# Performance work log

Hardware: AMD Instinct MI355X
Metric: run time of the kernel (lower is better)

The kernel has to match this reference:

```python
import jax, jax.numpy as jnp
import numpy as np

RADIUS = 400.0
FIELD = 8000.0  # um extent of slide coordinate field


def setup_inputs() -> dict:
    key = jax.random.key(0)
    ks = jax.random.split(key, 8)
    B, N, D, H, K = 4, 4096, 1536, 512, 8
    images = jax.random.normal(ks[0], (B, N, D), dtype=jnp.float32)
    positions = jax.random.uniform(ks[1], (B, N, 2), dtype=jnp.float32) * FIELD
    W_feat = jax.random.normal(ks[2], (D, H), dtype=jnp.float32) * (1.0 / np.sqrt(D))
    b_feat = jnp.zeros((H,), dtype=jnp.float32)
    W_pos = jax.random.normal(ks[3], (2, H), dtype=jnp.float32) * 0.5
    W_gnn = jax.random.normal(ks[4], (H, H), dtype=jnp.float32) * (1.0 / np.sqrt(H))
    W_self = jax.random.normal(ks[5], (H, H), dtype=jnp.float32) * (1.0 / np.sqrt(H))
    anchors = jax.random.normal(ks[6], (K, D), dtype=jnp.float32)
    return {"images": images, "positions": positions, "W_feat": W_feat,
            "b_feat": b_feat, "W_pos": W_pos, "W_gnn": W_gnn,
            "W_self": W_self, "anchors": anchors}


def _radius_adjacency(pos):
    # pos: (N, 2). Dense O(N^2) radius graph (mirrors torch.cdist + mask).
    sq = jnp.sum(pos * pos, axis=-1)                       # (N,)
    d2 = sq[:, None] + sq[None, :] - 2.0 * (pos @ pos.T)   # (N, N)
    mask = d2 < (RADIUS * RADIUS)
    N = pos.shape[0]
    mask = mask & ~jnp.eye(N, dtype=bool)                  # no self-loops
    return mask.astype(pos.dtype)


def reference(images, positions, W_feat, b_feat, W_pos, W_gnn, W_self, anchors):
    # --- Stream A: explicit concept quantifier (cosine sim to anchors) ---
    x_norm = images / jnp.clip(jnp.linalg.norm(images, axis=-1, keepdims=True), 1e-12)
    a_norm = anchors / jnp.clip(jnp.linalg.norm(anchors, axis=-1, keepdims=True), 1e-12)
    scores = jnp.einsum('bnd,kd->bnk', x_norm, a_norm)     # (B, N, K)
    concept_profile = scores.mean(axis=1)                  # (B, K)

    # --- Stream B: feature extraction with positional encoding ---
    feat = images @ W_feat + b_feat + positions @ W_pos    # (B, N, H)

    # --- radius graph + one mean-aggregation GNN layer, per slide ---
    def per_graph(f, p):
        A = _radius_adjacency(p)                           # (N, N)
        deg = jnp.clip(A.sum(axis=-1, keepdims=True), 1.0) # (N, 1)
        h = jax.nn.relu(f)
        agg = (A @ h) / deg                                # mean over neighbors
        return jax.nn.relu(agg @ W_gnn + f @ W_self)       # (N, H)

    refined = jax.vmap(per_graph)(feat, positions)         # (B, N, H)
    latent_spatial = refined.mean(axis=1)                  # (B, H)  per-graph mean pool

    return jnp.concatenate([latent_spatial, concept_profile], axis=1)  # (B, H+K)
```

## Files before the change

kernel.cpp:

```cpp
#include <hip/hip_runtime.h>

#define B_ 4
#define N_ 4096
#define D_ 1536
#define H_ 512
#define K_ 8
#define M_ (B_*N_)
#define R2_ 160000.0f
#define CAP 192

typedef __attribute__((ext_vector_type(8))) short bf16x8;
typedef __attribute__((ext_vector_type(4))) float f32x4;

__device__ __forceinline__ unsigned short f2bf(float f) {
  union { float f; unsigned u; } v; v.f = f;
  unsigned r = (v.u + 0x7FFFu + ((v.u >> 16) & 1u)) >> 16;
  return (unsigned short)r;
}

typedef const __attribute__((address_space(1))) unsigned int gas_u32;
typedef __attribute__((address_space(3))) unsigned int las_u32;
__device__ __forceinline__ void gl_lds16(const unsigned short* g, unsigned short* l) {
  __builtin_amdgcn_global_load_lds((gas_u32*)g, (las_u32*)l, 16, 0, 0);
}

__global__ __launch_bounds__(256) void k_prep(
    const float* __restrict__ Wf, const float* __restrict__ Wg, const float* __restrict__ Ws,
    const float* __restrict__ anchors, unsigned short* __restrict__ WfT,
    unsigned short* __restrict__ WgsT, float* __restrict__ anorm) {
  __shared__ float t[64][65];
  __shared__ float red[4];
  int bx = blockIdx.x, by = blockIdx.y, tid = threadIdx.x;
  if (by == 40) {
    int k = bx;
    float s = 0.f;
    for (int i = tid; i < D_; i += 256) { float v = anchors[k*D_ + i]; s += v*v; }
    #pragma unroll
    for (int off = 32; off; off >>= 1) s += __shfl_down(s, off);
    if ((tid & 63) == 0) red[tid >> 6] = s;
    __syncthreads();
    if (tid == 0) anorm[k] = fmaxf(sqrtf(red[0]+red[1]+red[2]+red[3]), 1e-12f);
    return;
  }
  const float* W; unsigned short* WT; int kt, outStride, outOff;
  if (by < 24)      { W = Wf; WT = WfT;  kt = by;      outStride = D_;   outOff = 0; }
  else if (by < 32) { W = Wg; WT = WgsT; kt = by - 24; outStride = 1024; outOff = 0; }
  else              { W = Ws; WT = WgsT; kt = by - 32; outStride = 1024; outOff = 512; }
  int tx = tid & 63, ty = tid >> 6;
  #pragma unroll
  for (int r = 0; r < 64; r += 4)
    t[ty + r][tx] = W[(size_t)(kt*64 + ty + r)*H_ + bx*64 + tx];
  __syncthreads();
  #pragma unroll
  for (int r = 0; r < 64; r += 4) {
    int n = bx*64 + ty + r;
    WT[(size_t)n*outStride + outOff + kt*64 + tx] = f2bf(t[tx][ty + r]);
  }
}

__global__ __launch_bounds__(256) void k_concept_cast(
    const float* __restrict__ images, const float* __restrict__ anchors,
    const float* __restrict__ anorm, unsigned short* __restrict__ imgs_bf,
    float* __restrict__ out) {
  __shared__ float sA[K_*D_];
  __shared__ float sc[4][K_];
  int tid = threadIdx.x, lane = tid & 63, w = tid >> 6;
  {
    const float4* a4 = (const float4*)anchors;
    float4* sA4 = (float4*)sA;
    #pragma unroll
    for (int i = 0; i < 12; i++) sA4[tid + 256*i] = a4[tid + 256*i];
  }
  __syncthreads();
  float acc_k[K_] = {};
  for (int r = 0; r < 8; r++) {
    int gm = blockIdx.x*32 + w*8 + r;
    const float4* xrow = (const float4*)(images + (size_t)gm*D_);
    float nrm = 0.f; float dot[K_] = {};
    #pragma unroll
    for (int it = 0; it < 6; it++) {
      int j = lane + 64*it;
      float4 x = xrow[j];
      nrm += x.x*x.x + x.y*x.y + x.z*x.z + x.w*x.w;
      #pragma unroll
      for (int k = 0; k < K_; k++) {
        float4 a = *(const float4*)&sA[(size_t)(k*384 + j)*4];
        dot[k] += x.x*a.x + x.y*a.y + x.z*a.z + x.w*a.w;
      }
      ushort4 s;
      s.x = f2bf(x.x); s.y = f2bf(x.y); s.z = f2bf(x.z); s.w = f2bf(x.w);
      *(ushort4*)&imgs_bf[(size_t)gm*D_ + (size_t)j*4] = s;
    }
    #pragma unroll
    for (int off = 32; off; off >>= 1) {
      nrm += __shfl_down(nrm, off);
      #pragma unroll
      for (int k = 0; k < K_; k++) dot[k] += __shfl_down(dot[k], off);
    }
    if (lane == 0) {
      float inv = 1.0f / fmaxf(sqrtf(nrm), 1e-12f);
      #pragma unroll
      for (int k = 0; k < K_; k++) acc_k[k] += dot[k] * inv / anorm[k];
    }
  }
  if (lane == 0) {
    #pragma unroll
    for (int k = 0; k < K_; k++) sc[w][k] = acc_k[k];
  }
  __syncthreads();
  if (tid < K_) {
    float s = sc[0][tid] + sc[1][tid] + sc[2][tid] + sc[3][tid];
    int b = blockIdx.x >> 7;
    atomicAdd(out + b*(H_+K_) + H_ + tid, s * (1.0f/N_));
  }
}

#define BM 128
#define BN 128
#define BK 32

__global__ __launch_bounds__(256) void k_gemm(
    const unsigned short* __restrict__ A, const unsigned short* __restrict__ BT,
    int Kdim, int mode, const float* __restrict__ bias, const float* __restrict__ Wpos,
    const float* __restrict__ positions, unsigned short* __restrict__ AB,
    float* __restrict__ out) {
  __shared__ unsigned short As[BM*BK];
  __shared__ unsigned short Bs[BN*BK];
  __shared__ float colsum[BN];
  int tid = threadIdx.x;
  int lane = tid & 63, wv = tid >> 6;
  int wm = wv >> 1, wn = wv & 1;
  int l15 = lane & 15, quad = lane >> 4;
  int bx = blockIdx.x;
  int bm = bx >> 2, bn = bx & 3;
  int m0 = bm*BM, n0 = bn*BN;

  f32x4 acc[4][4] = {};

  int c = wv*2;
  int rowc = (lane >> 2), seg = lane & 3;
  const unsigned short* gA0 = A  + (size_t)(m0 + c*16 + rowc)*Kdim + seg*8;
  const unsigned short* gA1 = gA0 + (size_t)16*Kdim;
  const unsigned short* gB0 = BT + (size_t)(n0 + c*16 + rowc)*Kdim + seg*8;
  const unsigned short* gB1 = gB0 + (size_t)16*Kdim;
  unsigned short* lA0 = As + c*512;
  unsigned short* lA1 = lA0 + 512;
  unsigned short* lB0 = Bs + c*512;
  unsigned short* lB1 = lB0 + 512;

  int nk = Kdim / BK;
  for (int kt = 0; kt < nk; kt++) {
    __syncthreads();
    gl_lds16(gA0, lA0); gl_lds16(gA1, lA1);
    gl_lds16(gB0, lB0); gl_lds16(gB1, lB1);
    gA0 += BK; gA1 += BK; gB0 += BK; gB1 += BK;
    __syncthreads();

    bf16x8 aF[4], bF[4];
    #pragma unroll
    for (int f = 0; f < 4; f++)
      aF[f] = *(const bf16x8*)&As[(wm*64 + f*16 + l15)*BK + quad*8];
    #pragma unroll
    for (int f = 0; f < 4; f++)
      bF[f] = *(const bf16x8*)&Bs[(wn*64 + f*16 + l15)*BK + quad*8];
    #pragma unroll
    for (int mi = 0; mi < 4; mi++)
      #pragma unroll
      for (int ni = 0; ni < 4; ni++)
        acc[mi][ni] = __builtin_amdgcn_mfma_f32_16x16x32_bf16(aF[mi], bF[ni], acc[mi][ni], 0, 0, 0);
  }

  if (mode == 0) {
    float bz[4], w0v[4], w1v[4];
    #pragma unroll
    for (int ni = 0; ni < 4; ni++) {
      int gh = n0 + wn*64 + ni*16 + l15;
      bz[ni] = bias[gh]; w0v[ni] = Wpos[gh]; w1v[ni] = Wpos[H_ + gh];
    }
    #pragma unroll
    for (int mi = 0; mi < 4; mi++) {
      #pragma unroll
      for (int r = 0; r < 4; r++) {
        int gm = m0 + wm*64 + mi*16 + quad*4 + r;
        float2 p = ((const float2*)positions)[gm];
        #pragma unroll
        for (int ni = 0; ni < 4; ni++) {
          int gh = n0 + wn*64 + ni*16 + l15;
          float v = acc[mi][ni][r] + bz[ni] + p.x*w0v[ni] + p.y*w1v[ni];
          AB[(size_t)gm*1024 + 512 + gh] = f2bf(v);
        }
      }
    }
  } else {
    if (tid < BN) colsum[tid] = 0.f;
    __syncthreads();
    #pragma unroll
    for (int ni = 0; ni < 4; ni++) {
      float s = 0.f;
      #pragma unroll
      for (int mi = 0; mi < 4; mi++) {
        #pragma unroll
        for (int r = 0; r < 4; r++) s += fmaxf(acc[mi][ni][r], 0.f);
      }
      s += __shfl_down(s, 32);
      s += __shfl_down(s, 16);
      if (quad == 0) atomicAdd(&colsum[wn*64 + ni*16 + l15], s);
    }
    __syncthreads();
    if (tid < BN) {
      int b = m0 >> 12;
      atomicAdd(out + b*(H_+K_) + n0 + tid, colsum[tid] * (1.0f/N_));
    }
  }
}

__global__ __launch_bounds__(256) void k_adjacency(const float* __restrict__ positions,
                                                   unsigned short* __restrict__ nlistG,
                                                   int* __restrict__ degG) {
  __shared__ float sdx[32], sdy[32];
  __shared__ int cnt[32];
  __shared__ unsigned short nl[32*CAP];
  int blk = blockIdx.x;
  int xcd = blk & 7;
  int b = xcd >> 1;
  int sub = ((blk >> 3) << 1) | (xcd & 1);
  int dest0 = sub * 32;
  int tid = threadIdx.x;
  const float2* p2 = (const float2*)(positions + (size_t)b*N_*2);
  if (tid < 32) {
    cnt[tid] = 0;
    float2 pd = p2[dest0 + tid];
    sdx[tid] = pd.x; sdy[tid] = pd.y;
  }
  __syncthreads();
  for (int it = 0; it < 16; it++) {
    int j = tid + 256*it;
    float2 pj = p2[j];
    #pragma unroll
    for (int d = 0; d < 32; d++) {
      float dx = pj.x - sdx[d], dy = pj.y - sdy[d];
      if (dx*dx + dy*dy < R2_ && j != dest0 + d) {
        int p = atomicAdd(&cnt[d], 1);
        if (p < CAP) nl[d*CAP + p] = (unsigned short)j;
      }
    }
  }
  __syncthreads();
  int gd0 = (b << 12) + dest0;
  uint4* dst = (uint4*)(nlistG + (size_t)gd0*CAP);
  const uint4* src = (const uint4*)nl;
  #pragma unroll
  for (int i = 0; i < 3; i++) dst[tid + 256*i] = src[tid + 256*i];
  if (tid < 32) degG[gd0 + tid] = min(cnt[tid], CAP);
}

__device__ __forceinline__ void acc8(uint4 v, float* a) {
  union { unsigned u; float f; } t;
  t.u = v.x << 16;          a[0] += fmaxf(t.f, 0.f);
  t.u = v.x & 0xFFFF0000u;  a[1] += fmaxf(t.f, 0.f);
  t.u = v.y << 16;          a[2] += fmaxf(t.f, 0.f);
  t.u = v.y & 0xFFFF0000u;  a[3] += fmaxf(t.f, 0.f);
  t.u = v.z << 16;          a[4] += fmaxf(t.f, 0.f);
  t.u = v.z & 0xFFFF0000u;  a[5] += fmaxf(t.f, 0.f);
  t.u = v.w << 16;          a[6] += fmaxf(t.f, 0.f);
  t.u = v.w & 0xFFFF0000u;  a[7] += fmaxf(t.f, 0.f);
}

__global__ __launch_bounds__(256) void k_aggregate(const unsigned short* __restrict__ nlistG,
                                                   const int* __restrict__ degG,
                                                   unsigned short* __restrict__ AB) {
  __shared__ unsigned short nl[8*CAP];
  __shared__ int dg[8];
  int blk = blockIdx.x;
  int xcd = blk & 7;
  int b = xcd >> 1;
  int sub = ((blk >> 3) << 1) | (xcd & 1);
  int dest0 = sub * 8;
  int gd0 = (b << 12) + dest0;
  int tid = threadIdx.x, lane = tid & 63, w = tid >> 6;
  if (tid < 192) ((uint4*)nl)[tid] = ((const uint4*)(nlistG + (size_t)gd0*CAP))[tid];
  if (tid < 8) dg[tid] = degG[gd0 + tid];
  __syncthreads();
  const unsigned short* featb = AB + ((size_t)(b << 12))*1024 + 512 + lane*8;
  #pragma unroll
  for (int dd = 0; dd < 2; dd++) {
    int d = w*2 + dd;
    int deg = dg[d];
    float inv = 1.0f / (float)(deg > 1 ? deg : 1);
    const unsigned short* nlp = &nl[d*CAP];
    float a[8] = {};
    int n = 0;
    for (; n + 4 <= deg; n += 4) {
      ushort4 idx = *(const ushort4*)&nlp[n];
      uint4 v0 = *(const uint4*)(featb + (size_t)idx.x*1024);
      uint4 v1 = *(const uint4*)(featb + (size_t)idx.y*1024);
      uint4 v2 = *(const uint4*)(featb + (size_t)idx.z*1024);
      uint4 v3 = *(const uint4*)(featb + (size_t)idx.w*1024);
      acc8(v0, a); acc8(v1, a); acc8(v2, a); acc8(v3, a);
    }
    for (; n < deg; n++) {
      int j = nlp[n];
      uint4 v = *(const uint4*)(featb + (size_t)j*1024);
      acc8(v, a);
    }
    uint4 o;
    o.x = ((unsigned)f2bf(a[1]*inv) << 16) | f2bf(a[0]*inv);
    o.y = ((unsigned)f2bf(a[3]*inv) << 16) | f2bf(a[2]*inv);
    o.z = ((unsigned)f2bf(a[5]*inv) << 16) | f2bf(a[4]*inv);
    o.w = ((unsigned)f2bf(a[7]*inv) << 16) | f2bf(a[6]*inv);
    *(uint4*)(AB + (size_t)(gd0 + d)*1024 + lane*8) = o;
  }
}

extern "C" void kernel_launch(void* const* d_in, const int* in_sizes, int n_in,
                              void* d_out, int out_size, void* d_ws, size_t ws_size,
                              hipStream_t stream) {
  const float* images    = (const float*)d_in[0];
  const float* positions = (const float*)d_in[1];
  const float* W_feat    = (const float*)d_in[2];
  const float* b_feat    = (const float*)d_in[3];
  const float* W_pos     = (const float*)d_in[4];
  const float* W_gnn     = (const float*)d_in[5];
  const float* W_self    = (const float*)d_in[6];
  const float* anchors   = (const float*)d_in[7];
  float* out = (float*)d_out;

  char* ws = (char*)d_ws;
  unsigned short* imgs_bf = (unsigned short*)ws;
  unsigned short* nlistG  = (unsigned short*)ws;
  int*            degG    = (int*)(ws + 6291456);
  unsigned short* AB      = (unsigned short*)(ws + 50331648);
  unsigned short* WfT     = (unsigned short*)(ws + 83886080);
  unsigned short* WgsT    = (unsigned short*)(ws + 85458944);
  float*          anorm   = (float*)(ws + 86507520);

  hipMemsetAsync(d_out, 0, sizeof(float)*B_*(H_+K_), stream);
  k_prep<<<dim3(8, 41), 256, 0, stream>>>(W_feat, W_gnn, W_self, anchors, WfT, WgsT, anorm);
  k_concept_cast<<<M_/32, 256, 0, stream>>>(images, anchors, anorm, imgs_bf, out);
  k_gemm<<<512, 256, 0, stream>>>(imgs_bf, WfT, D_, 0, b_feat, W_pos, positions, AB, out);
  k_adjacency<<<512, 256, 0, stream>>>(positions, nlistG, degG);
  k_aggregate<<<2048, 256, 0, stream>>>(nlistG, degG, AB);
  k_gemm<<<512, 256, 0, stream>>>(AB, WgsT, 1024, 1, nullptr, nullptr, nullptr, AB, out);
}
```

Before: 327.5 us.

## Fuse concept scoring and bf16 cast into first GEMM reading fp32 images

Removes the separate concept/cast kernel and its bf16 image buffer. The first GEMM now loads fp32 image tiles into LDS with an XOR swizzle, converts them to bf16 in registers for MFMA, and uses an extra fifth column-block per row tile to compute the norms and anchor dot products. Blocks are remapped so each XCD handles a contiguous M range, and the second GEMM is specialized the same way. The fp32 A tiles double LDS traffic, and every image row is read once per N-block (five times), which replaces the single read plus bf16 write and reread of the old path.

```diff
diff --git a/kernel.cpp b/kernel.cpp
--- a/kernel.cpp
+++ b/kernel.cpp
@@ -20,7 +20,7 @@
 
 typedef const __attribute__((address_space(1))) unsigned int gas_u32;
 typedef __attribute__((address_space(3))) unsigned int las_u32;
-__device__ __forceinline__ void gl_lds16(const unsigned short* g, unsigned short* l) {
+__device__ __forceinline__ void gl_lds16(const void* g, void* l) {
   __builtin_amdgcn_global_load_lds((gas_u32*)g, (las_u32*)l, 16, 0, 0);
 }
 
@@ -58,119 +58,125 @@
   }
 }
 
-__global__ __launch_bounds__(256) void k_concept_cast(
-    const float* __restrict__ images, const float* __restrict__ anchors,
-    const float* __restrict__ anorm, unsigned short* __restrict__ imgs_bf,
+#define BM 128
+#define BK 32
+
+__global__ __launch_bounds__(256) void k_gemm1f(
+    const float* __restrict__ images, const unsigned short* __restrict__ WfT,
+    const float* __restrict__ bias, const float* __restrict__ Wpos,
+    const float* __restrict__ positions, const float* __restrict__ anchors,
+    const float* __restrict__ anorm, unsigned short* __restrict__ AB,
     float* __restrict__ out) {
-  __shared__ float sA[K_*D_];
-  __shared__ float sc[4][K_];
-  int tid = threadIdx.x, lane = tid & 63, w = tid >> 6;
-  {
-    const float4* a4 = (const float4*)anchors;
-    float4* sA4 = (float4*)sA;
-    #pragma unroll
-    for (int i = 0; i < 12; i++) sA4[tid + 256*i] = a4[tid + 256*i];
-  }
-  __syncthreads();
-  float acc_k[K_] = {};
-  for (int r = 0; r < 8; r++) {
-    int gm = blockIdx.x*32 + w*8 + r;
-    const float4* xrow = (const float4*)(images + (size_t)gm*D_);
-    float nrm = 0.f; float dot[K_] = {};
-    #pragma unroll
-    for (int it = 0; it < 6; it++) {
-      int j = lane + 64*it;
-      float4 x = xrow[j];
-      nrm += x.x*x.x + x.y*x.y + x.z*x.z + x.w*x.w;
-      #pragma unroll
-      for (int k = 0; k < K_; k++) {
-        float4 a = *(const float4*)&sA[(size_t)(k*384 + j)*4];
-        dot[k] += x.x*a.x + x.y*a.y + x.z*a.z + x.w*a.w;
-      }
-      ushort4 s;
-      s.x = f2bf(x.x); s.y = f2bf(x.y); s.z = f2bf(x.z); s.w = f2bf(x.w);
-      *(ushort4*)&imgs_bf[(size_t)gm*D_ + (size_t)j*4] = s;
-    }
-    #pragma unroll
-    for (int off = 32; off; off >>= 1) {
-      nrm += __shfl_down(nrm, off);
-      #pragma unroll
-      for (int k = 0; k < K_; k++) dot[k] += __shfl_down(dot[k], off);
-    }
-    if (lane == 0) {
-      float inv = 1.0f / fmaxf(sqrtf(nrm), 1e-12f);
-      #pragma unroll
-      for (int k = 0; k < K_; k++) acc_k[k] += dot[k] * inv / anorm[k];
-    }
-  }
-  if (lane == 0) {
-    #pragma unroll
-    for (int k = 0; k < K_; k++) sc[w][k] = acc_k[k];
-  }
-  __syncthreads();
-  if (tid < K_) {
-    float s = sc[0][tid] + sc[1][tid] + sc[2][tid] + sc[3][tid];
-    int b = blockIdx.x >> 7;
-    atomicAdd(out + b*(H_+K_) + H_ + tid, s * (1.0f/N_));
-  }
-}
-
-#define BM 128
-#define BN 128
-#define BK 32
-
-__global__ __launch_bounds__(256) void k_gemm(
-    const unsigned short* __restrict__ A, const unsigned short* __restrict__ BT,
-    int Kdim, int mode, const float* __restrict__ bias, const float* __restrict__ Wpos,
-    const float* __restrict__ positions, unsigned short* __restrict__ AB,
-    float* __restrict__ out) {
-  __shared__ unsigned short As[BM*BK];
-  __shared__ unsigned short Bs[BN*BK];
-  __shared__ float colsum[BN];
-  int tid = threadIdx.x;
-  int lane = tid & 63, wv = tid >> 6;
-  int wm = wv >> 1, wn = wv & 1;
+  __shared__ float Asf[BM*BK];
+  __shared__ unsigned short Bsh[12288];
+  __shared__ float sConc[8];
+  int tid = threadIdx.x, lane = tid & 63, wv = tid >> 6;
   int l15 = lane & 15, quad = lane >> 4;
   int bx = blockIdx.x;
-  int bm = bx >> 2, bn = bx & 3;
-  int m0 = bm*BM, n0 = bn*BN;
+  int xcd = bx & 7, idx = bx >> 3;
+  int q5 = idx / 5;
+  int bm = xcd*16 + q5, bn = idx - q5*5;
+  int m0 = bm*BM;
+  bool isC = (bn == 4);
+  int n0 = bn*128;
+
+  int r8 = lane >> 3, qp = (lane & 7) >> 1, rem = (lane & 1)*4;
+  int lw = ((qp ^ (r8 & 3)) << 3) + rem;
+  const float* gA = images + (size_t)(m0 + wv*32 + r8)*D_ + lw;
+  float* lA = Asf + wv*32*BK;
+
+  const unsigned short* gB = WfT + (size_t)(n0 + wv*32 + (lane >> 2))*D_ + (lane & 3)*8;
+  unsigned short* lB = Bsh + wv*32*BK;
+
+  if (isC) {
+    for (int i = tid; i < 3072; i += 256) {
+      float4 a = ((const float4*)anchors)[i];
+      ushort4 s; s.x = f2bf(a.x); s.y = f2bf(a.y); s.z = f2bf(a.z); s.w = f2bf(a.w);
+      ((ushort4*)Bsh)[i] = s;
+    }
+  }
+  if (tid < 8) sConc[tid] = 0.f;
 
   f32x4 acc[4][4] = {};
-
-  int c = wv*2;
-  int rowc = (lane >> 2), seg = lane & 3;
-  const unsigned short* gA0 = A  + (size_t)(m0 + c*16 + rowc)*Kdim + seg*8;
-  const unsigned short* gA1 = gA0 + (size_t)16*Kdim;
-  const unsigned short* gB0 = BT + (size_t)(n0 + c*16 + rowc)*Kdim + seg*8;
-  const unsigned short* gB1 = gB0 + (size_t)16*Kdim;
-  unsigned short* lA0 = As + c*512;
-  unsigned short* lA1 = lA0 + 512;
-  unsigned short* lB0 = Bs + c*512;
-  unsigned short* lB1 = lB0 + 512;
-
-  int nk = Kdim / BK;
-  for (int kt = 0; kt < nk; kt++) {
-    __syncthreads();
-    gl_lds16(gA0, lA0); gl_lds16(gA1, lA1);
-    gl_lds16(gB0, lB0); gl_lds16(gB1, lB1);
-    gA0 += BK; gA1 += BK; gB0 += BK; gB1 += BK;
-    __syncthreads();
-
-    bf16x8 aF[4], bF[4];
-    #pragma unroll
-    for (int f = 0; f < 4; f++)
-      aF[f] = *(const bf16x8*)&As[(wm*64 + f*16 + l15)*BK + quad*8];
-    #pragma unroll
-    for (int f = 0; f < 4; f++)
-      bF[f] = *(const bf16x8*)&Bs[(wn*64 + f*16 + l15)*BK + quad*8];
-    #pragma unroll
-    for (int mi = 0; mi < 4; mi++)
-      #pragma unroll
-      for (int ni = 0; ni < 4; ni++)
-        acc[mi][ni] = __builtin_amdgcn_mfma_f32_16x16x32_bf16(aF[mi], bF[ni], acc[mi][ni], 0, 0, 0);
-  }
-
-  if (mode == 0) {
+  float dk[8] = {};
+  float ss = 0.f;
+  int wm = wv >> 1, wn = wv & 1;
+  int crow = tid >> 1, ch = tid & 1;
+  int cs0 = (((2*ch)   ^ (crow & 3)) << 3);
+  int cs1 = (((2*ch+1) ^ (crow & 3)) << 3);
+  const float* crp = &Asf[crow*BK];
+
+  for (int kt = 0; kt < 48; kt++) {
+    __syncthreads();
+    #pragma unroll
+    for (int t = 0; t < 4; t++)
+      gl_lds16(gA + (size_t)t*8*D_, lA + t*8*BK);
+    if (!isC) {
+      gl_lds16(gB, lB);
+      gl_lds16(gB + (size_t)16*D_, lB + 16*BK);
+    }
+    gA += BK; gB += BK;
+    __syncthreads();
+
+    if (!isC) {
+      bf16x8 aF[4], bF[4];
+      #pragma unroll
+      for (int f = 0; f < 4; f++) {
+        int row = wm*64 + f*16 + l15;
+        const float* ap = &Asf[row*BK + ((quad ^ (row & 3)) << 3)];
+        float4 x0 = *(const float4*)ap;
+        float4 x1 = *(const float4*)(ap + 4);
+        bf16x8 v;
+        v[0] = f2bf(x0.x); v[1] = f2bf(x0.y); v[2] = f2bf(x0.z); v[3] = f2bf(x0.w);
+        v[4] = f2bf(x1.x); v[5] = f2bf(x1.y); v[6] = f2bf(x1.z); v[7] = f2bf(x1.w);
+        aF[f] = v;
+      }
+      #pragma unroll
+      for (int f = 0; f < 4; f++)
+        bF[f] = *(const bf16x8*)&Bsh[(wn*64 + f*16 + l15)*BK + quad*8];
+      #pragma unroll
+      for (int mi = 0; mi < 4; mi++)
+        #pragma unroll
+        for (int ni = 0; ni < 4; ni++)
+          acc[mi][ni] = __builtin_amdgcn_mfma_f32_16x16x32_bf16(aF[mi], bF[ni], acc[mi][ni], 0, 0, 0);
+    } else {
+      float4 x0 = *(const float4*)(crp + cs0);
+      float4 x1 = *(const float4*)(crp + cs0 + 4);
+      float4 x2 = *(const float4*)(crp + cs1);
+      float4 x3 = *(const float4*)(crp + cs1 + 4);
+      ss += x0.x*x0.x + x0.y*x0.y + x0.z*x0.z + x0.w*x0.w
+          + x1.x*x1.x + x1.y*x1.y + x1.z*x1.z + x1.w*x1.w
+          + x2.x*x2.x + x2.y*x2.y + x2.z*x2.z + x2.w*x2.w
+          + x3.x*x3.x + x3.y*x3.y + x3.z*x3.z + x3.w*x3.w;
+      const unsigned short* abase = &Bsh[kt*32 + ch*16];
+      #pragma unroll
+      for (int k = 0; k < 8; k++) {
+        uint4 a0 = *(const uint4*)(abase + (size_t)k*D_);
+        uint4 a1 = *(const uint4*)(abase + (size_t)k*D_ + 8);
+        union { unsigned u; float f; } c;
+        float s = 0.f;
+        c.u = a0.x << 16;         s += x0.x*c.f;
+        c.u = a0.x & 0xFFFF0000u; s += x0.y*c.f;
+        c.u = a0.y << 16;         s += x0.z*c.f;
+        c.u = a0.y & 0xFFFF0000u; s += x0.w*c.f;
+        c.u = a0.z << 16;         s += x1.x*c.f;
+        c.u = a0.z & 0xFFFF0000u; s += x1.y*c.f;
+        c.u = a0.w << 16;         s += x1.z*c.f;
+        c.u = a0.w & 0xFFFF0000u; s += x1.w*c.f;
+        c.u = a1.x << 16;         s += x2.x*c.f;
+        c.u = a1.x & 0xFFFF0000u; s += x2.y*c.f;
+        c.u = a1.y << 16;         s += x2.z*c.f;
+        c.u = a1.y & 0xFFFF0000u; s += x2.w*c.f;
+        c.u = a1.z << 16;         s += x3.x*c.f;
+        c.u = a1.z & 0xFFFF0000u; s += x3.y*c.f;
+        c.u = a1.w << 16;         s += x3.z*c.f;
+        c.u = a1.w & 0xFFFF0000u; s += x3.w*c.f;
+        dk[k] += s;
+      }
+    }
+  }
+
+  if (!isC) {
     float bz[4], w0v[4], w1v[4];
     #pragma unroll
     for (int ni = 0; ni < 4; ni++) {
@@ -192,25 +198,86 @@
       }
     }
   } else {
-    if (tid < BN) colsum[tid] = 0.f;
-    __syncthreads();
-    #pragma unroll
-    for (int ni = 0; ni < 4; ni++) {
-      float s = 0.f;
-      #pragma unroll
-      for (int mi = 0; mi < 4; mi++) {
-        #pragma unroll
-        for (int r = 0; r < 4; r++) s += fmaxf(acc[mi][ni][r], 0.f);
-      }
-      s += __shfl_down(s, 32);
-      s += __shfl_down(s, 16);
-      if (quad == 0) atomicAdd(&colsum[wn*64 + ni*16 + l15], s);
-    }
-    __syncthreads();
-    if (tid < BN) {
-      int b = m0 >> 12;
-      atomicAdd(out + b*(H_+K_) + n0 + tid, colsum[tid] * (1.0f/N_));
-    }
+    #pragma unroll
+    for (int k = 0; k < 8; k++) dk[k] += __shfl_xor(dk[k], 1);
+    ss += __shfl_xor(ss, 1);
+    if (ch == 0) {
+      float inv = 1.0f / fmaxf(sqrtf(ss), 1e-12f);
+      #pragma unroll
+      for (int k = 0; k < 8; k++) atomicAdd(&sConc[k], dk[k]*inv / anorm[k]);
+    }
+    __syncthreads();
+    if (tid < 8) atomicAdd(out + (m0 >> 12)*(H_+K_) + H_ + tid, sConc[tid]*(1.0f/N_));
+  }
+}
+
+__global__ __launch_bounds__(256) void k_gemm2(
+    const unsigned short* __restrict__ A, const unsigned short* __restrict__ BT,
+    float* __restrict__ out) {
+  __shared__ unsigned short As[BM*BK];
+  __shared__ unsigned short Bs[128*BK];
+  __shared__ float colsum[128];
+  int tid = threadIdx.x;
+  int lane = tid & 63, wv = tid >> 6;
+  int wm = wv >> 1, wn = wv & 1;
+  int l15 = lane & 15, quad = lane >> 4;
+  int bx = blockIdx.x;
+  int xcd = bx & 7, idx = bx >> 3;
+  int bm = xcd*16 + (idx >> 2), bn = idx & 3;
+  int m0 = bm*BM, n0 = bn*128;
+
+  f32x4 acc[4][4] = {};
+
+  int c = wv*2;
+  int rowc = (lane >> 2), seg = lane & 3;
+  const unsigned short* gA0 = A + (size_t)(m0 + c*16 + rowc)*1024 + seg*8;
+  const unsigned short* gA1 = gA0 + (size_t)16*1024;
+  const unsigned short* gB0 = BT + (size_t)(n0 + c*16 + rowc)*1024 + seg*8;
+  const unsigned short* gB1 = gB0 + (size_t)16*1024;
+  unsigned short* lA0 = As + c*512;
+  unsigned short* lA1 = lA0 + 512;
+  unsigned short* lB0 = Bs + c*512;
+  unsigned short* lB1 = lB0 + 512;
+
+  for (int kt = 0; kt < 32; kt++) {
+    __syncthreads();
+    gl_lds16(gA0, lA0); gl_lds16(gA1, lA1);
+    gl_lds16(gB0, lB0); gl_lds16(gB1, lB1);
+    gA0 += BK; gA1 += BK; gB0 += BK; gB1 += BK;
+    __syncthreads();
+
+    bf16x8 aF[4], bF[4];
+    #pragma unroll
+    for (int f = 0; f < 4; f++)
+      aF[f] = *(const bf16x8*)&As[(wm*64 + f*16 + l15)*BK + quad*8];
+    #pragma unroll
+    for (int f = 0; f < 4; f++)
+      bF[f] = *(const bf16x8*)&Bs[(wn*64 + f*16 + l15)*BK + quad*8];
+    #pragma unroll
+    for (int mi = 0; mi < 4; mi++)
+      #pragma unroll
+      for (int ni = 0; ni < 4; ni++)
+        acc[mi][ni] = __builtin_amdgcn_mfma_f32_16x16x32_bf16(aF[mi], bF[ni], acc[mi][ni], 0, 0, 0);
+  }
+
+  if (tid < 128) colsum[tid] = 0.f;
+  __syncthreads();
+  #pragma unroll
+  for (int ni = 0; ni < 4; ni++) {
+    float s = 0.f;
+    #pragma unroll
+    for (int mi = 0; mi < 4; mi++) {
+      #pragma unroll
+      for (int r = 0; r < 4; r++) s += fmaxf(acc[mi][ni][r], 0.f);
+    }
+    s += __shfl_down(s, 32);
+    s += __shfl_down(s, 16);
+    if (quad == 0) atomicAdd(&colsum[wn*64 + ni*16 + l15], s);
+  }
+  __syncthreads();
+  if (tid < 128) {
+    int b = m0 >> 12;
+    atomicAdd(out + b*(H_+K_) + n0 + tid, colsum[tid] * (1.0f/N_));
   }
 }
 
@@ -326,7 +393,6 @@
   float* out = (float*)d_out;
 
   char* ws = (char*)d_ws;
-  unsigned short* imgs_bf = (unsigned short*)ws;
   unsigned short* nlistG  = (unsigned short*)ws;
   int*            degG    = (int*)(ws + 6291456);
   unsigned short* AB      = (unsigned short*)(ws + 50331648);
@@ -336,9 +402,8 @@
 
   hipMemsetAsync(d_out, 0, sizeof(float)*B_*(H_+K_), stream);
   k_prep<<<dim3(8, 41), 256, 0, stream>>>(W_feat, W_gnn, W_self, anchors, WfT, WgsT, anorm);
-  k_concept_cast<<<M_/32, 256, 0, stream>>>(images, anchors, anorm, imgs_bf, out);
-  k_gemm<<<512, 256, 0, stream>>>(imgs_bf, WfT, D_, 0, b_feat, W_pos, positions, AB, out);
+  k_gemm1f<<<640, 256, 0, stream>>>(images, WfT, b_feat, W_pos, positions, anchors, anorm, AB, out);
   k_adjacency<<<512, 256, 0, stream>>>(positions, nlistG, degG);
   k_aggregate<<<2048, 256, 0, stream>>>(nlistG, degG, AB);
-  k_gemm<<<512, 256, 0, stream>>>(AB, WgsT, 1024, 1, nullptr, nullptr, nullptr, AB, out);
-}
+  k_gemm2<<<512, 256, 0, stream>>>(AB, WgsT, out);
+}
```

Result: slower. 384.8 us (+17.5%).
